# Kernel tuning notes

Measured on AMD Instinct MI355X. Metric: run time of the kernel, lower is better.

Reference implementation:

```python
import jax, jax.numpy as jnp
import numpy as np

D_G = 16384; B = 128; NNZ = 262144
CL1_F = 32; CL1_K = 6; FC1_F = 512; FC2_F = 512
NN_FC1 = 512; NN_FC2 = 256
CL4_F = 32; CL4_K = 4; FC1_G4 = 128; FC2_G4 = 64
OUT = 10; POOL1 = 8; POOL4 = 3; V4 = 10; EMB = 64
FC1FIN = CL1_F * (D_G // POOL1)        # 65536
G4OUT = CL4_F * (OUT // POOL4)         # 96
SUMFIN = FC1_F + NN_FC2 + FC2_G4 + 64  # 896


def _cheby(x, W, b, spmm, K):
    # x: [B, V, Fin]; Chebyshev recursion T_k(L) x with K-order feature stacking
    Bb, V, Fin = x.shape
    x0 = jnp.transpose(x, (1, 2, 0)).reshape(V, Fin * Bb)
    xs = [x0]
    if K > 1:
        x1 = spmm(x0)
        xs.append(x1)
        for _ in range(K - 2):
            x2 = 2.0 * spmm(x1) - x0
            xs.append(x2)
            x0, x1 = x1, x2
    X = jnp.stack(xs).reshape(K, V, Fin, Bb)
    X = jnp.transpose(X, (3, 1, 2, 0)).reshape(Bb * V, Fin * K)  # [B*V, Fin*K]
    return (X @ W.T + b).reshape(Bb, V, -1)


def _gmaxpool(x, p):
    # MaxPool1d(p) over node dim (floor truncation like torch)
    Bb, V, F = x.shape
    Vp = (V // p) * p
    return x[:, :Vp].reshape(Bb, V // p, p, F).max(axis=2)


def setup_inputs():
    key = jax.random.key(0)
    ks = jax.random.split(key, 32)
    def lin(i, fo, fi):
        return (jax.random.normal(ks[i], (fo, fi), jnp.float32) * 0.02,
                jnp.zeros((fo,), jnp.float32))
    cl1_W, cl1_b = lin(0, CL1_F, CL1_K)
    fc1_W, fc1_b = lin(1, FC1_F, FC1FIN)
    fc2_W, fc2_b = lin(2, FC2_F, FC1_F)
    fc3_W, fc3_b = lin(3, D_G, FC2_F)
    nn1_W, nn1_b = lin(4, NN_FC1, D_G)
    nn2_W, nn2_b = lin(5, NN_FC2, NN_FC1)
    cl4_W, cl4_b = lin(6, CL4_F, CL4_K * EMB)
    fcg1_W, fcg1_b = lin(7, FC1_G4, G4OUT)
    fcg2_W, fcg2_b = lin(8, FC2_G4, FC1_G4)
    nn14_W, nn14_b = lin(9, 256, V4 * EMB)
    nn24_W, nn24_b = lin(10, 64, 256)
    fcsum_W, fcsum_b = lin(11, OUT, SUMFIN)
    return {
        'x_in': jax.random.normal(ks[12], (B, D_G), jnp.float32),
        'x_embed': jax.random.normal(ks[13], (V4, EMB), jnp.float32),
        'dropout': 0,
        'L_rows': jnp.sort(jax.random.randint(ks[14], (NNZ,), 0, D_G)),
        'L_cols': jax.random.randint(ks[15], (NNZ,), 0, D_G),
        'L_vals': jax.random.normal(ks[16], (NNZ,), jnp.float32) * 0.1,
        'L_mg': jax.random.normal(ks[17], (V4, V4), jnp.float32) * 0.2,
        'cl1_W': cl1_W, 'cl1_b': cl1_b, 'fc1_W': fc1_W, 'fc1_b': fc1_b,
        'fc2_W': fc2_W, 'fc2_b': fc2_b, 'fc3_W': fc3_W, 'fc3_b': fc3_b,
        'nn1_W': nn1_W, 'nn1_b': nn1_b, 'nn2_W': nn2_W, 'nn2_b': nn2_b,
        'cl4_W': cl4_W, 'cl4_b': cl4_b, 'fcg1_W': fcg1_W, 'fcg1_b': fcg1_b,
        'fcg2_W': fcg2_W, 'fcg2_b': fcg2_b, 'nn14_W': nn14_W, 'nn14_b': nn14_b,
        'nn24_W': nn24_W, 'nn24_b': nn24_b, 'fcsum_W': fcsum_W, 'fcsum_b': fcsum_b,
    }


def reference(x_in, x_embed, dropout, L_rows, L_cols, L_vals, L_mg,
              cl1_W, cl1_b, fc1_W, fc1_b, fc2_W, fc2_b, fc3_W, fc3_b,
              nn1_W, nn1_b, nn2_W, nn2_b, cl4_W, cl4_b,
              fcg1_W, fcg1_b, fcg2_W, fcg2_b, nn14_W, nn14_b, nn24_W, nn24_b,
              fcsum_W, fcsum_b):
    Bb = x_in.shape[0]
    def spmm_L(m):  # COO SpMM: y[r] += v * m[c]
        return jax.ops.segment_sum(L_vals[:, None] * m[L_cols], L_rows,
                                   num_segments=D_G)
    # --- GCN 1 (gene graph) ---
    x = _cheby(x_in[:, :, None], cl1_W, cl1_b, spmm_L, CL1_K)
    x = jax.nn.relu(x)
    x = _gmaxpool(x, POOL1).reshape(Bb, FC1FIN)
    x_hidden_gae = jax.nn.relu(x @ fc1_W.T + fc1_b)
    # FC2_F != 0 branch; dropout p=0 is identity at this baseline
    x_decode_gae = jax.nn.relu(x_hidden_gae @ fc2_W.T + fc2_b)
    x_decode_gae = x_decode_gae @ fc3_W.T + fc3_b
    # --- NN 1 ---
    x_nn = jax.nn.relu(x_in @ nn1_W.T + nn1_b)
    x_nn = jax.nn.relu(x_nn @ nn2_W.T + nn2_b)
    # --- GCN 4 (small meta-graph, dense Laplacian) ---
    xe = jnp.broadcast_to(x_embed[None], (Bb, V4, EMB))
    xg = _cheby(xe, cl4_W, cl4_b, lambda m: L_mg @ m, CL4_K)
    xg = jax.nn.relu(xg)
    xg = _gmaxpool(xg, POOL4).reshape(Bb, G4OUT)
    xg = jax.nn.relu(xg @ fcg1_W.T + fcg1_b)
    xg = jax.nn.relu(xg @ fcg2_W.T + fcg2_b)
    # --- NN of GCN4 ---
    xn4 = xe.reshape(Bb, V4 * EMB)
    xn4 = jax.nn.relu(xn4 @ nn14_W.T + nn14_b)
    xn4 = jax.nn.relu(xn4 @ nn24_W.T + nn24_b)
    data_emb = jnp.concatenate([x_hidden_gae, x_nn, xg, xn4], axis=1)
    logp = jax.nn.log_softmax(data_emb @ fcsum_W.T + fcsum_b, axis=-1)
    return x_decode_gae, x_hidden_gae, logp
```

## Files before the change

### kernel.cpp

```cpp
#include <hip/hip_runtime.h>
#include <hip/hip_bf16.h>

#define DG 16384
#define NNZ 262144
#define BB 128

typedef __attribute__((ext_vector_type(8))) short bf16x8;
typedef __attribute__((ext_vector_type(8))) unsigned short us8;
typedef __attribute__((ext_vector_type(4))) float f32x4;
typedef __attribute__((ext_vector_type(4))) unsigned short us4;
typedef __attribute__((ext_vector_type(2))) float f32x2;

#define WS_ROWPTR 0
#define WS_XIN16  66048
#define WS_T      4260352
#define WS_XPOOL  54592000
#define WS_XB0    71369216
#define WS_XB1    75563520
#define WS_XNN1B  79757824
#define WS_DEC2   79888896
#define WS_XNN2   80019968
#define WS_HIDB   80151040
#define WS_N1     80282112
#define WS_TAIL   80283136
#define PART_NN1_OFF 0
#define PART_FC1_OFF 8388608

__device__ __forceinline__ unsigned short f2bf(float f) {
  __hip_bfloat16 h = __float2bfloat16(f);
  return __builtin_bit_cast(unsigned short, h);
}
__device__ __forceinline__ float bflo(unsigned u) {
  return __builtin_bit_cast(float, u << 16);
}
__device__ __forceinline__ float bfhi(unsigned u) {
  return __builtin_bit_cast(float, u & 0xffff0000u);
}

__device__ void prep_dev(const float* __restrict__ x_in, const int* __restrict__ rows,
                         int* __restrict__ rowptr, unsigned short* __restrict__ xin16,
                         int bid) {
  int idx = bid * 256 + threadIdx.x;
  if (idx <= DG) {
    int lo = 0, hi = NNZ;
    while (lo < hi) { int mid = (lo + hi) >> 1; if (rows[mid] < idx) lo = mid + 1; else hi = mid; }
    rowptr[idx] = lo;
  }
  f32x4 v = ((const f32x4*)x_in)[idx];
  us4 o; o[0] = f2bf(v[0]); o[1] = f2bf(v[1]); o[2] = f2bf(v[2]); o[3] = f2bf(v[3]);
  ((us4*)xin16)[idx] = o;
}

__device__ void transpose_dev(const float* __restrict__ x_in, float* __restrict__ T0,
                              unsigned short* __restrict__ Xb0, int id) {
  __shared__ float tl[32][33];
  int bx = id & 511, by = id >> 9;
  int v0 = bx * 32, b0 = by * 32;
  int tx = threadIdx.x & 31, ty0 = threadIdx.x >> 5;
  #pragma unroll
  for (int j = 0; j < 4; ++j) {
    int ty = ty0 + j * 8;
    tl[ty][tx] = x_in[(size_t)(b0 + ty) * DG + v0 + tx];
  }
  __syncthreads();
  #pragma unroll
  for (int j = 0; j < 4; ++j) {
    int ty = ty0 + j * 8;
    float v = tl[tx][ty];
    size_t o = (size_t)(v0 + ty) * BB + b0 + tx;
    T0[o] = v;
    Xb0[o] = f2bf(v);
  }
}

__device__ void dot4_dev(const float* __restrict__ x, const float* __restrict__ W,
                         const float* __restrict__ bias, float* __restrict__ out,
                         int K, int id) {
  int w = threadIdx.x >> 6, lane = threadIdx.x & 63;
  int o = id * 4 + w;
  float a = 0.f;
  for (int i = lane; i < K; i += 64) a += x[i] * W[(size_t)o * K + i];
  #pragma unroll
  for (int s = 32; s > 0; s >>= 1) a += __shfl_down(a, s);
  if (lane == 0) out[o] = fmaxf(a + bias[o], 0.f);
}

__device__ void g4_dev(const float* __restrict__ xe_g, const float* __restrict__ Lmg_g,
                       const float* __restrict__ W4, const float* __restrict__ b4,
                       const float* __restrict__ Wg1, const float* __restrict__ bg1,
                       const float* __restrict__ Wg2, const float* __restrict__ bg2,
                       float* __restrict__ tail) {
  __shared__ float Lm[100], Tg[4][640], xc[320], xg96[96], h1[128];
  int t = threadIdx.x;
  for (int i = t; i < 640; i += 256) Tg[0][i] = xe_g[i];
  for (int i = t; i < 100; i += 256) Lm[i] = Lmg_g[i];
  __syncthreads();
  for (int i = t; i < 640; i += 256) {
    int v = i >> 6, f = i & 63; float s = 0.f;
    #pragma unroll
    for (int u = 0; u < 10; ++u) s += Lm[v * 10 + u] * Tg[0][u * 64 + f];
    Tg[1][i] = s;
  }
  __syncthreads();
  for (int kk = 2; kk < 4; ++kk) {
    for (int i = t; i < 640; i += 256) {
      int v = i >> 6, f = i & 63; float s = 0.f;
      #pragma unroll
      for (int u = 0; u < 10; ++u) s += Lm[v * 10 + u] * Tg[kk - 1][u * 64 + f];
      Tg[kk][i] = 2.f * s - Tg[kk - 2][i];
    }
    __syncthreads();
  }
  for (int i = t; i < 320; i += 256) {
    int v = i >> 5, fo = i & 31; float s = b4[fo];
    for (int fin = 0; fin < 64; ++fin)
      #pragma unroll
      for (int k = 0; k < 4; ++k) s += Tg[k][v * 64 + fin] * W4[fo * 256 + fin * 4 + k];
    xc[i] = fmaxf(s, 0.f);
  }
  __syncthreads();
  for (int i = t; i < 96; i += 256) {
    int g = i >> 5, fo = i & 31;
    xg96[i] = fmaxf(fmaxf(xc[(3 * g) * 32 + fo], xc[(3 * g + 1) * 32 + fo]),
                    xc[(3 * g + 2) * 32 + fo]);
  }
  __syncthreads();
  for (int o = t; o < 128; o += 256) {
    float s = bg1[o];
    for (int i2 = 0; i2 < 96; ++i2) s += xg96[i2] * Wg1[o * 96 + i2];
    h1[o] = fmaxf(s, 0.f);
  }
  __syncthreads();
  for (int o = t; o < 64; o += 256) {
    float s = bg2[o];
    for (int i2 = 0; i2 < 128; ++i2) s += h1[i2] * Wg2[o * 128 + i2];
    tail[o] = fmaxf(s, 0.f);
  }
}

__global__ __launch_bounds__(256) void setup_kernel(
    const float* __restrict__ x_in, const int* __restrict__ rows,
    int* __restrict__ rowptr, unsigned short* __restrict__ xin16,
    float* __restrict__ T0, unsigned short* __restrict__ Xb0,
    const float* __restrict__ x_embed,
    const float* __restrict__ nn14_W, const float* __restrict__ nn14_b,
    float* __restrict__ n1,
    const float* __restrict__ Lmg, const float* __restrict__ W4,
    const float* __restrict__ b4, const float* __restrict__ Wg1,
    const float* __restrict__ bg1, const float* __restrict__ Wg2,
    const float* __restrict__ bg2, float* __restrict__ tail) {
  int bid = blockIdx.x;
  if (bid < 2048) prep_dev(x_in, rows, rowptr, xin16, bid);
  else if (bid < 4096) transpose_dev(x_in, T0, Xb0, bid - 2048);
  else if (bid < 4160) dot4_dev(x_embed, nn14_W, nn14_b, n1, 640, bid - 4096);
  else g4_dev(x_embed, Lmg, W4, b4, Wg1, bg1, Wg2, bg2, tail);
}

__global__ __launch_bounds__(256) void spmm3(
    const int* __restrict__ rowptr, const int* __restrict__ cols,
    const float* __restrict__ vals, const unsigned* __restrict__ X2,
    const float* __restrict__ Tprev, float* __restrict__ Tout,
    unsigned* __restrict__ Xbout, float scale) {
  int r = blockIdx.x * 4 + (threadIdx.x >> 6);
  int lane = threadIdx.x & 63;
  int e0 = rowptr[r], e1 = rowptr[r + 1];
  float a00 = 0.f, a01 = 0.f, a10 = 0.f, a11 = 0.f;
  int e = e0;
  for (; e + 4 <= e1; e += 4) {
    int c0 = cols[e], c1 = cols[e + 1], c2 = cols[e + 2], c3 = cols[e + 3];
    float v0 = vals[e], v1 = vals[e + 1], v2 = vals[e + 2], v3 = vals[e + 3];
    unsigned x0 = X2[c0 * 64 + lane], x1 = X2[c1 * 64 + lane];
    unsigned x2 = X2[c2 * 64 + lane], x3 = X2[c3 * 64 + lane];
    a00 += v0 * bflo(x0); a10 += v0 * bfhi(x0);
    a01 += v1 * bflo(x1); a11 += v1 * bfhi(x1);
    a00 += v2 * bflo(x2); a10 += v2 * bfhi(x2);
    a01 += v3 * bflo(x3); a11 += v3 * bfhi(x3);
  }
  for (; e < e1; ++e) {
    float v = vals[e]; unsigned x = X2[cols[e] * 64 + lane];
    a00 += v * bflo(x); a10 += v * bfhi(x);
  }
  float s0 = scale * (a00 + a01), s1 = scale * (a10 + a11);
  size_t o = (size_t)r * BB + lane * 2;
  if (Tprev) { f32x2 p = *(const f32x2*)(Tprev + o); s0 -= p[0]; s1 -= p[1]; }
  *(f32x2*)(Tout + o) = (f32x2){s0, s1};
  Xbout[(size_t)r * 64 + lane] = (unsigned)f2bf(s0) | ((unsigned)f2bf(s1) << 16);
}

__device__ void combine_dev(const float* __restrict__ Tbase, const float* __restrict__ W,
                            const float* __restrict__ bias, unsigned short* __restrict__ xpool,
                            int vp) {
  __shared__ float tile[6][8][128];
  __shared__ float Wl[192];
  __shared__ float bl[32];
  for (int i = threadIdx.x; i < 192; i += 256) Wl[i] = W[i];
  if (threadIdx.x < 32) bl[threadIdx.x] = bias[threadIdx.x];
  for (int i = threadIdx.x; i < 6144; i += 256) {
    int k = i >> 10, rem = i & 1023, j = rem >> 7, b = rem & 127;
    tile[k][j][b] = Tbase[(size_t)k * 2097152 + (size_t)(vp * 8 + j) * BB + b];
  }
  __syncthreads();
  for (int p = threadIdx.x; p < 4096; p += 256) {
    int b = p >> 5, f = p & 31;
    float m = -1e30f;
    #pragma unroll
    for (int j = 0; j < 8; ++j) {
      float s = bl[f];
      #pragma unroll
      for (int k = 0; k < 6; ++k) s += tile[k][j][b] * Wl[f * 6 + k];
      m = fmaxf(m, s);
    }
    m = fmaxf(m, 0.f);
    xpool[(size_t)b * 65536 + vp * 32 + f] = f2bf(m);
  }
}

__global__ __launch_bounds__(256) void combine_nn24(
    const float* __restrict__ Tbase, const float* __restrict__ W,
    const float* __restrict__ bias, unsigned short* __restrict__ xpool,
    const float* __restrict__ n1, const float* __restrict__ nn24_W,
    const float* __restrict__ nn24_b, float* __restrict__ tail64) {
  int bid = blockIdx.x;
  if (bid < 2048) combine_dev(Tbase, W, bias, xpool, bid);
  else dot4_dev(n1, nn24_W, nn24_b, tail64, 256, bid - 2048);
}

template<int NT>
__device__ void gemm_core(
    unsigned short* __restrict__ Alds,
    unsigned short* __restrict__ Wlds,
    const unsigned short* __restrict__ A, const float* __restrict__ W,
    float* __restrict__ outP, unsigned short* __restrict__ outB,
    const float* __restrict__ bias, int K, int N, int Kchunk,
    int bx, int by, int relu, int partial) {
  const int CN = NT * 64;
  int t = threadIdx.x, w = t >> 6, lane = t & 63, lr = lane & 15, lg = lane >> 4;
  int n0 = bx * CN;
  int kbeg = by * Kchunk;
  f32x4 acc[8][NT];
  #pragma unroll
  for (int mt = 0; mt < 8; ++mt)
    #pragma unroll
    for (int nt = 0; nt < NT; ++nt)
      acc[mt][nt] = (f32x4){0.f, 0.f, 0.f, 0.f};
  int stages = Kchunk >> 6;
  for (int s = 0; s < stages; ++s) {
    int k0 = kbeg + s * 64;
    #pragma unroll
    for (int j = 0; j < 4; ++j) {
      int idx = j * 256 + t;
      int row = idx >> 3, kk = (idx & 7) * 8;
      us8 v = *(const us8*)(A + (size_t)row * K + k0 + kk);
      *(us8*)(Alds + row * 64 + (kk ^ ((row & 7) << 3))) = v;
    }
    #pragma unroll
    for (int j = 0; j < NT * 4; ++j) {
      int idx = j * 256 + t;
      int wr = idx >> 4, kk = (idx & 15) * 4;
      f32x4 v = *(const f32x4*)(W + (size_t)(n0 + wr) * K + k0 + kk);
      us4 o; o[0] = f2bf(v[0]); o[1] = f2bf(v[1]); o[2] = f2bf(v[2]); o[3] = f2bf(v[3]);
      *(us4*)(Wlds + wr * 64 + (kk ^ ((wr & 7) << 3))) = o;
    }
    __syncthreads();
    #pragma unroll
    for (int h = 0; h < 2; ++h) {
      int k32 = h * 32;
      bf16x8 bfr[NT];
      #pragma unroll
      for (int nt = 0; nt < NT; ++nt) {
        int wrow = w * NT * 16 + nt * 16 + lr;
        bfr[nt] = *(const bf16x8*)(Wlds + wrow * 64 + ((k32 + lg * 8) ^ ((wrow & 7) << 3)));
      }
      #pragma unroll
      for (int mt = 0; mt < 8; ++mt) {
        int arow = mt * 16 + lr;
        bf16x8 af = *(const bf16x8*)(Alds + arow * 64 + ((k32 + lg * 8) ^ ((arow & 7) << 3)));
        #pragma unroll
        for (int nt = 0; nt < NT; ++nt)
          acc[mt][nt] = __builtin_amdgcn_mfma_f32_16x16x32_bf16(af, bfr[nt], acc[mt][nt], 0, 0, 0);
      }
    }
    __syncthreads();
  }
  if (partial) {
    float* P = outP + (size_t)by * 128 * (size_t)N;
    #pragma unroll
    for (int mt = 0; mt < 8; ++mt)
      #pragma unroll
      for (int nt = 0; nt < NT; ++nt) {
        int col = n0 + w * NT * 16 + nt * 16 + lr;
        #pragma unroll
        for (int r2 = 0; r2 < 4; ++r2) {
          int row = mt * 16 + lg * 4 + r2;
          P[(size_t)row * N + col] = acc[mt][nt][r2];
        }
      }
  } else {
    #pragma unroll
    for (int mt = 0; mt < 8; ++mt)
      #pragma unroll
      for (int nt = 0; nt < NT; ++nt) {
        int col = n0 + w * NT * 16 + nt * 16 + lr;
        float bc = bias[col];
        #pragma unroll
        for (int r2 = 0; r2 < 4; ++r2) {
          int row = mt * 16 + lg * 4 + r2;
          float v = acc[mt][nt][r2] + bc;
          if (relu) v = fmaxf(v, 0.f);
          if (outP) outP[(size_t)row * N + col] = v;
          if (outB) outB[(size_t)row * N + col] = f2bf(v);
        }
      }
  }
}

__global__ __launch_bounds__(256) void gemm_partials(
    const unsigned short* __restrict__ xin16, const float* __restrict__ nn1_W,
    const unsigned short* __restrict__ xpool, const float* __restrict__ fc1_W,
    float* __restrict__ pnn1, float* __restrict__ pfc1) {
  __shared__ unsigned short Alds[128 * 64];
  __shared__ unsigned short Wlds[128 * 64];
  int b = blockIdx.x;
  if (b < 128)
    gemm_core<2>(Alds, Wlds, xin16, nn1_W, pnn1, nullptr, nullptr,
                 16384, 512, 512, b & 3, b >> 2, 0, 1);
  else {
    b -= 128;
    gemm_core<2>(Alds, Wlds, xpool, fc1_W, pfc1, nullptr, nullptr,
                 65536, 512, 512, b & 3, b >> 2, 0, 1);
  }
}

__global__ __launch_bounds__(256) void reduce_fused(
    const float* __restrict__ pfc1, const float* __restrict__ fc1_b,
    float* __restrict__ hidden, unsigned short* __restrict__ hidB,
    const float* __restrict__ pnn1, const float* __restrict__ nn1_b,
    unsigned short* __restrict__ xnn1b) {
  int b = blockIdx.x;
  if (b < 256) {
    int idx = b * 256 + threadIdx.x;
    float s = 0.f;
    for (int i = 0; i < 128; ++i) s += pfc1[(size_t)i * 65536 + idx];
    float v = fmaxf(s + fc1_b[idx & 511], 0.f);
    hidden[idx] = v;
    hidB[idx] = f2bf(v);
  } else {
    int idx = (b - 256) * 256 + threadIdx.x;
    float s = 0.f;
    for (int i = 0; i < 32; ++i) s += pnn1[(size_t)i * 65536 + idx];
    float v = fmaxf(s + nn1_b[idx & 511], 0.f);
    xnn1b[idx] = f2bf(v);
  }
}

__global__ __launch_bounds__(256) void fc2nn2_kernel(
    const unsigned short* __restrict__ hidB, const float* __restrict__ fc2_W,
    const float* __restrict__ fc2_b, unsigned short* __restrict__ dec2,
    const unsigned short* __restrict__ xnn1b, const float* __restrict__ nn2_W,
    const float* __restrict__ nn2_b, float* __restrict__ xnn2) {
  __shared__ unsigned short Alds[128 * 64];
  __shared__ unsigned short Wlds[64 * 64];
  int b = blockIdx.x;
  if (b < 8)
    gemm_core<1>(Alds, Wlds, hidB, fc2_W, nullptr, dec2, fc2_b,
                 512, 512, 512, b, 0, 1, 0);
  else
    gemm_core<1>(Alds, Wlds, xnn1b, nn2_W, xnn2, nullptr, nn2_b,
                 512, 256, 512, b - 8, 0, 1, 0);
}

__device__ void fcsum_dev(int id, const float* __restrict__ hidden,
                          const float* __restrict__ xnn2, const float* __restrict__ tail,
                          const float* __restrict__ Ws, const float* __restrict__ bs,
                          float* __restrict__ logp) {
  __shared__ float emb[4][896];
  int w = threadIdx.x >> 6, lane = threadIdx.x & 63;
  int b = id * 4 + w;
  for (int i = lane; i < 896; i += 64)
    emb[w][i] = (i < 512) ? hidden[b * 512 + i]
              : (i < 768) ? xnn2[b * 256 + (i - 512)]
                          : tail[i - 768];
  float l[10];
  #pragma unroll
  for (int o = 0; o < 10; ++o) {
    float a = 0.f;
    for (int i = lane; i < 896; i += 64) a += emb[w][i] * Ws[o * 896 + i];
    #pragma unroll
    for (int s = 32; s > 0; s >>= 1) a += __shfl_down(a, s);
    l[o] = __shfl(a, 0) + bs[o];
  }
  float m = l[0];
  #pragma unroll
  for (int o = 1; o < 10; ++o) m = fmaxf(m, l[o]);
  float sum = 0.f;
  #pragma unroll
  for (int o = 0; o < 10; ++o) sum += expf(l[o] - m);
  float lse = m + logf(sum);
  #pragma unroll
  for (int o = 0; o < 10; ++o)
    if (lane == o) logp[b * 10 + o] = l[o] - lse;
}

__global__ __launch_bounds__(256) void fc3_head(
    const unsigned short* __restrict__ dec2, const float* __restrict__ fc3_W,
    const float* __restrict__ fc3_b, float* __restrict__ out0,
    const float* __restrict__ hidden, const float* __restrict__ xnn2,
    const float* __restrict__ tail, const float* __restrict__ fcsum_W,
    const float* __restrict__ fcsum_b, float* __restrict__ logp) {
  __shared__ unsigned short Alds[128 * 64];
  __shared__ unsigned short Wlds[64 * 64];
  int b = blockIdx.x;
  if (b < 256)
    gemm_core<1>(Alds, Wlds, dec2, fc3_W, out0, nullptr, fc3_b,
                 512, 16384, 512, b, 0, 0, 0);
  else
    fcsum_dev(b - 256, hidden, xnn2, tail, fcsum_W, fcsum_b, logp);
}

extern "C" void kernel_launch(void* const* d_in, const int* in_sizes, int n_in,
                              void* d_out, int out_size, void* d_ws, size_t ws_size,
                              hipStream_t stream) {
  const float* x_in    = (const float*)d_in[0];
  const float* x_embed = (const float*)d_in[1];
  const int*   L_rows  = (const int*)d_in[3];
  const int*   L_cols  = (const int*)d_in[4];
  const float* L_vals  = (const float*)d_in[5];
  const float* L_mg    = (const float*)d_in[6];
  const float* cl1_W = (const float*)d_in[7],  *cl1_b = (const float*)d_in[8];
  const float* fc1_W = (const float*)d_in[9],  *fc1_b = (const float*)d_in[10];
  const float* fc2_W = (const float*)d_in[11], *fc2_b = (const float*)d_in[12];
  const float* fc3_W = (const float*)d_in[13], *fc3_b = (const float*)d_in[14];
  const float* nn1_W = (const float*)d_in[15], *nn1_b = (const float*)d_in[16];
  const float* nn2_W = (const float*)d_in[17], *nn2_b = (const float*)d_in[18];
  const float* cl4_W = (const float*)d_in[19], *cl4_b = (const float*)d_in[20];
  const float* fcg1_W = (const float*)d_in[21], *fcg1_b = (const float*)d_in[22];
  const float* fcg2_W = (const float*)d_in[23], *fcg2_b = (const float*)d_in[24];
  const float* nn14_W = (const float*)d_in[25], *nn14_b = (const float*)d_in[26];
  const float* nn24_W = (const float*)d_in[27], *nn24_b = (const float*)d_in[28];
  const float* fcsum_W = (const float*)d_in[29], *fcsum_b = (const float*)d_in[30];

  char* ws = (char*)d_ws;
  int* rowptr = (int*)(ws + WS_ROWPTR);
  unsigned short* xin16 = (unsigned short*)(ws + WS_XIN16);
  float* T = (float*)(ws + WS_T);
  unsigned short* xpool = (unsigned short*)(ws + WS_XPOOL);
  unsigned short* Xb0 = (unsigned short*)(ws + WS_XB0);
  unsigned short* Xb1 = (unsigned short*)(ws + WS_XB1);
  unsigned short* xnn1b = (unsigned short*)(ws + WS_XNN1B);
  unsigned short* dec2 = (unsigned short*)(ws + WS_DEC2);
  float* xnn2 = (float*)(ws + WS_XNN2);
  unsigned short* hidB = (unsigned short*)(ws + WS_HIDB);
  float* n1 = (float*)(ws + WS_N1);
  float* tail = (float*)(ws + WS_TAIL);
  float* pnn1 = (float*)(ws + WS_T + PART_NN1_OFF);
  float* pfc1 = (float*)(ws + WS_T + PART_FC1_OFF);

  float* out0 = (float*)d_out;
  float* hidden = out0 + 2097152;
  float* logp = out0 + 2097152 + 65536;

  setup_kernel<<<4161, 256, 0, stream>>>(x_in, L_rows, rowptr, xin16, T, Xb0,
                                         x_embed, nn14_W, nn14_b, n1,
                                         L_mg, cl4_W, cl4_b, fcg1_W, fcg1_b,
                                         fcg2_W, fcg2_b, tail);

  spmm3<<<4096, 256, 0, stream>>>(rowptr, L_cols, L_vals, (const unsigned*)Xb0,
                                  nullptr,          T + 1 * 2097152, (unsigned*)Xb1, 1.f);
  spmm3<<<4096, 256, 0, stream>>>(rowptr, L_cols, L_vals, (const unsigned*)Xb1,
                                  T,                T + 2 * 2097152, (unsigned*)Xb0, 2.f);
  spmm3<<<4096, 256, 0, stream>>>(rowptr, L_cols, L_vals, (const unsigned*)Xb0,
                                  T + 1 * 2097152,  T + 3 * 2097152, (unsigned*)Xb1, 2.f);
  spmm3<<<4096, 256, 0, stream>>>(rowptr, L_cols, L_vals, (const unsigned*)Xb1,
                                  T + 2 * 2097152,  T + 4 * 2097152, (unsigned*)Xb0, 2.f);
  spmm3<<<4096, 256, 0, stream>>>(rowptr, L_cols, L_vals, (const unsigned*)Xb0,
                                  T + 3 * 2097152,  T + 5 * 2097152, (unsigned*)Xb1, 2.f);

  combine_nn24<<<2064, 256, 0, stream>>>(T, cl1_W, cl1_b, xpool,
                                         n1, nn24_W, nn24_b, tail + 64);

  gemm_partials<<<640, 256, 0, stream>>>(xin16, nn1_W, xpool, fc1_W, pnn1, pfc1);

  reduce_fused<<<512, 256, 0, stream>>>(pfc1, fc1_b, hidden, hidB,
                                        pnn1, nn1_b, xnn1b);

  fc2nn2_kernel<<<12, 256, 0, stream>>>(hidB, fc2_W, fc2_b, dec2,
                                        xnn1b, nn2_W, nn2_b, xnn2);

  fc3_head<<<288, 256, 0, stream>>>(dec2, fc3_W, fc3_b, out0,
                                    hidden, xnn2, tail, fcsum_W, fcsum_b, logp);
}
```

Baseline: 257.7 us.

## Pre-convert weights to bf16 in spare blocks and register-prefetch GEMM tiles

```diff
diff --git a/kernel.cpp b/kernel.cpp
--- a/kernel.cpp
+++ b/kernel.cpp
@@ -25,6 +25,11 @@
 #define WS_TAIL   80283136
 #define PART_NN1_OFF 0
 #define PART_FC1_OFF 8388608
+#define WS_NN1W16 81000448
+#define WS_FC3W16 97777664
+#define WS_FC2W16 114554880
+#define WS_NN2W16 115079168
+#define WS_FC1W16 115341312
 
 __device__ __forceinline__ unsigned short f2bf(float f) {
   __hip_bfloat16 h = __float2bfloat16(f);
@@ -35,6 +40,17 @@
 }
 __device__ __forceinline__ float bfhi(unsigned u) {
   return __builtin_bit_cast(float, u & 0xffff0000u);
+}
+
+__device__ void conv_dev(const float* __restrict__ src,
+                         unsigned short* __restrict__ dst, int id) {
+  #pragma unroll
+  for (int j = 0; j < 8; ++j) {
+    size_t el = (size_t)id * 8192 + j * 1024 + threadIdx.x * 4;
+    f32x4 v = *(const f32x4*)(src + el);
+    us4 o; o[0] = f2bf(v[0]); o[1] = f2bf(v[1]); o[2] = f2bf(v[2]); o[3] = f2bf(v[3]);
+    *(us4*)(dst + el) = o;
+  }
 }
 
 __device__ void prep_dev(const float* __restrict__ x_in, const int* __restrict__ rows,
@@ -148,19 +164,27 @@
     const float* __restrict__ Lmg, const float* __restrict__ W4,
     const float* __restrict__ b4, const float* __restrict__ Wg1,
     const float* __restrict__ bg1, const float* __restrict__ Wg2,
-    const float* __restrict__ bg2, float* __restrict__ tail) {
+    const float* __restrict__ bg2, float* __restrict__ tail,
+    const float* __restrict__ nn1_W, unsigned short* __restrict__ nn1w16,
+    const float* __restrict__ fc2_W, unsigned short* __restrict__ fc2w16,
+    const float* __restrict__ nn2_W, unsigned short* __restrict__ nn2w16) {
   int bid = blockIdx.x;
-  if (bid < 2048) prep_dev(x_in, rows, rowptr, xin16, bid);
-  else if (bid < 4096) transpose_dev(x_in, T0, Xb0, bid - 2048);
-  else if (bid < 4160) dot4_dev(x_embed, nn14_W, nn14_b, n1, 640, bid - 4096);
-  else g4_dev(x_embed, Lmg, W4, b4, Wg1, bg1, Wg2, bg2, tail);
+  if (bid < 1) g4_dev(x_embed, Lmg, W4, b4, Wg1, bg1, Wg2, bg2, tail);
+  else if (bid < 65) dot4_dev(x_embed, nn14_W, nn14_b, n1, 640, bid - 1);
+  else if (bid < 2113) prep_dev(x_in, rows, rowptr, xin16, bid - 65);
+  else if (bid < 4161) transpose_dev(x_in, T0, Xb0, bid - 2113);
+  else if (bid < 5185) conv_dev(nn1_W, nn1w16, bid - 4161);
+  else if (bid < 5217) conv_dev(fc2_W, fc2w16, bid - 5185);
+  else conv_dev(nn2_W, nn2w16, bid - 5217);
 }
 
 __global__ __launch_bounds__(256) void spmm3(
     const int* __restrict__ rowptr, const int* __restrict__ cols,
     const float* __restrict__ vals, const unsigned* __restrict__ X2,
     const float* __restrict__ Tprev, float* __restrict__ Tout,
-    unsigned* __restrict__ Xbout, float scale) {
+    unsigned* __restrict__ Xbout, float scale,
+    const float* __restrict__ csrc, unsigned short* __restrict__ cdst) {
+  if (blockIdx.x >= 4096) { conv_dev(csrc, cdst, blockIdx.x - 4096); return; }
   int r = blockIdx.x * 4 + (threadIdx.x >> 6);
   int lane = threadIdx.x & 63;
   int e0 = rowptr[r], e1 = rowptr[r + 1];
@@ -225,41 +249,53 @@
   else dot4_dev(n1, nn24_W, nn24_b, tail64, 256, bid - 2048);
 }
 
-template<int NT>
-__device__ void gemm_core(
+template<int NT, int MT>
+__device__ void gemm_core2(
     unsigned short* __restrict__ Alds,
     unsigned short* __restrict__ Wlds,
-    const unsigned short* __restrict__ A, const float* __restrict__ W,
+    const unsigned short* __restrict__ A, const unsigned short* __restrict__ W,
     float* __restrict__ outP, unsigned short* __restrict__ outB,
     const float* __restrict__ bias, int K, int N, int Kchunk,
-    int bx, int by, int relu, int partial) {
-  const int CN = NT * 64;
+    int bx, int by, int row0, int relu, int partial) {
+  const int LA = (MT * 16) / 32;
+  const int LW = (NT * 64) / 32;
   int t = threadIdx.x, w = t >> 6, lane = t & 63, lr = lane & 15, lg = lane >> 4;
-  int n0 = bx * CN;
+  int n0 = bx * NT * 64;
   int kbeg = by * Kchunk;
-  f32x4 acc[8][NT];
-  #pragma unroll
-  for (int mt = 0; mt < 8; ++mt)
-    #pragma unroll
-    for (int nt = 0; nt < NT; ++nt)
-      acc[mt][nt] = (f32x4){0.f, 0.f, 0.f, 0.f};
+  f32x4 acc[MT][NT];
+  #pragma unroll
+  for (int mt = 0; mt < MT; ++mt)
+    #pragma unroll
+    for (int nt = 0; nt < NT; ++nt) acc[mt][nt] = (f32x4){0.f, 0.f, 0.f, 0.f};
+  int rowA[LA], kkA[LA], rowW[LW], kkW[LW];
+  #pragma unroll
+  for (int j = 0; j < LA; ++j) { int idx = j * 256 + t; rowA[j] = idx >> 3; kkA[j] = (idx & 7) * 8; }
+  #pragma unroll
+  for (int j = 0; j < LW; ++j) { int idx = j * 256 + t; rowW[j] = idx >> 3; kkW[j] = (idx & 7) * 8; }
+  us8 ra[LA], rw[LW];
+  #pragma unroll
+  for (int j = 0; j < LA; ++j)
+    ra[j] = *(const us8*)(A + (size_t)(row0 + rowA[j]) * K + kbeg + kkA[j]);
+  #pragma unroll
+  for (int j = 0; j < LW; ++j)
+    rw[j] = *(const us8*)(W + (size_t)(n0 + rowW[j]) * K + kbeg + kkW[j]);
   int stages = Kchunk >> 6;
   for (int s = 0; s < stages; ++s) {
-    int k0 = kbeg + s * 64;
-    #pragma unroll
-    for (int j = 0; j < 4; ++j) {
-      int idx = j * 256 + t;
-      int row = idx >> 3, kk = (idx & 7) * 8;
-      us8 v = *(const us8*)(A + (size_t)row * K + k0 + kk);
-      *(us8*)(Alds + row * 64 + (kk ^ ((row & 7) << 3))) = v;
-    }
-    #pragma unroll
-    for (int j = 0; j < NT * 4; ++j) {
-      int idx = j * 256 + t;
-      int wr = idx >> 4, kk = (idx & 15) * 4;
-      f32x4 v = *(const f32x4*)(W + (size_t)(n0 + wr) * K + k0 + kk);
-      us4 o; o[0] = f2bf(v[0]); o[1] = f2bf(v[1]); o[2] = f2bf(v[2]); o[3] = f2bf(v[3]);
-      *(us4*)(Wlds + wr * 64 + (kk ^ ((wr & 7) << 3))) = o;
+    __syncthreads();
+    #pragma unroll
+    for (int j = 0; j < LA; ++j)
+      *(us8*)(Alds + rowA[j] * 64 + (kkA[j] ^ ((rowA[j] & 7) << 3))) = ra[j];
+    #pragma unroll
+    for (int j = 0; j < LW; ++j)
+      *(us8*)(Wlds + rowW[j] * 64 + (kkW[j] ^ ((rowW[j] & 7) << 3))) = rw[j];
+    if (s + 1 < stages) {
+      int k0 = kbeg + (s + 1) * 64;
+      #pragma unroll
+      for (int j = 0; j < LA; ++j)
+        ra[j] = *(const us8*)(A + (size_t)(row0 + rowA[j]) * K + k0 + kkA[j]);
+      #pragma unroll
+      for (int j = 0; j < LW; ++j)
+        rw[j] = *(const us8*)(W + (size_t)(n0 + rowW[j]) * K + k0 + kkW[j]);
     }
     __syncthreads();
     #pragma unroll
@@ -272,7 +308,7 @@
         bfr[nt] = *(const bf16x8*)(Wlds + wrow * 64 + ((k32 + lg * 8) ^ ((wrow & 7) << 3)));
       }
       #pragma unroll
-      for (int mt = 0; mt < 8; ++mt) {
+      for (int mt = 0; mt < MT; ++mt) {
         int arow = mt * 16 + lr;
         bf16x8 af = *(const bf16x8*)(Alds + arow * 64 + ((k32 + lg * 8) ^ ((arow & 7) << 3)));
         #pragma unroll
@@ -280,31 +316,30 @@
           acc[mt][nt] = __builtin_amdgcn_mfma_f32_16x16x32_bf16(af, bfr[nt], acc[mt][nt], 0, 0, 0);
       }
     }
-    __syncthreads();
   }
   if (partial) {
     float* P = outP + (size_t)by * 128 * (size_t)N;
     #pragma unroll
-    for (int mt = 0; mt < 8; ++mt)
+    for (int mt = 0; mt < MT; ++mt)
       #pragma unroll
       for (int nt = 0; nt < NT; ++nt) {
         int col = n0 + w * NT * 16 + nt * 16 + lr;
         #pragma unroll
         for (int r2 = 0; r2 < 4; ++r2) {
-          int row = mt * 16 + lg * 4 + r2;
+          int row = row0 + mt * 16 + lg * 4 + r2;
           P[(size_t)row * N + col] = acc[mt][nt][r2];
         }
       }
   } else {
     #pragma unroll
-    for (int mt = 0; mt < 8; ++mt)
+    for (int mt = 0; mt < MT; ++mt)
       #pragma unroll
       for (int nt = 0; nt < NT; ++nt) {
         int col = n0 + w * NT * 16 + nt * 16 + lr;
         float bc = bias[col];
         #pragma unroll
         for (int r2 = 0; r2 < 4; ++r2) {
-          int row = mt * 16 + lg * 4 + r2;
+          int row = row0 + mt * 16 + lg * 4 + r2;
           float v = acc[mt][nt][r2] + bc;
           if (relu) v = fmaxf(v, 0.f);
           if (outP) outP[(size_t)row * N + col] = v;
@@ -315,19 +350,21 @@
 }
 
 __global__ __launch_bounds__(256) void gemm_partials(
-    const unsigned short* __restrict__ xin16, const float* __restrict__ nn1_W,
-    const unsigned short* __restrict__ xpool, const float* __restrict__ fc1_W,
+    const unsigned short* __restrict__ xin16, const unsigned short* __restrict__ nn1w16,
+    const unsigned short* __restrict__ xpool, const unsigned short* __restrict__ fc1w16,
     float* __restrict__ pnn1, float* __restrict__ pfc1) {
   __shared__ unsigned short Alds[128 * 64];
   __shared__ unsigned short Wlds[128 * 64];
-  int b = blockIdx.x;
-  if (b < 128)
-    gemm_core<2>(Alds, Wlds, xin16, nn1_W, pnn1, nullptr, nullptr,
-                 16384, 512, 512, b & 3, b >> 2, 0, 1);
-  else {
-    b -= 128;
-    gemm_core<2>(Alds, Wlds, xpool, fc1_W, pfc1, nullptr, nullptr,
-                 65536, 512, 512, b & 3, b >> 2, 0, 1);
+  int nb = blockIdx.x;
+  if (nb < 128) {
+    int xcd = nb & 7, q = nb >> 3, bx = q & 3, by = ((q >> 2) << 3) | xcd;
+    gemm_core2<2, 8>(Alds, Wlds, xin16, nn1w16, pnn1, nullptr, nullptr,
+                     16384, 512, 512, bx, by, 0, 0, 1);
+  } else {
+    int b = nb - 128;
+    int xcd = b & 7, q = b >> 3, bx = q & 3, by = ((q >> 2) << 3) | xcd;
+    gemm_core2<2, 8>(Alds, Wlds, xpool, fc1w16, pfc1, nullptr, nullptr,
+                     65536, 512, 512, bx, by, 0, 0, 1);
   }
 }
 
@@ -354,19 +391,19 @@
 }
 
 __global__ __launch_bounds__(256) void fc2nn2_kernel(
-    const unsigned short* __restrict__ hidB, const float* __restrict__ fc2_W,
+    const unsigned short* __restrict__ hidB, const unsigned short* __restrict__ fc2w16,
     const float* __restrict__ fc2_b, unsigned short* __restrict__ dec2,
-    const unsigned short* __restrict__ xnn1b, const float* __restrict__ nn2_W,
+    const unsigned short* __restrict__ xnn1b, const unsigned short* __restrict__ nn2w16,
     const float* __restrict__ nn2_b, float* __restrict__ xnn2) {
   __shared__ unsigned short Alds[128 * 64];
   __shared__ unsigned short Wlds[64 * 64];
   int b = blockIdx.x;
   if (b < 8)
-    gemm_core<1>(Alds, Wlds, hidB, fc2_W, nullptr, dec2, fc2_b,
-                 512, 512, 512, b, 0, 1, 0);
+    gemm_core2<1, 8>(Alds, Wlds, hidB, fc2w16, nullptr, dec2, fc2_b,
+                     512, 512, 512, b, 0, 0, 1, 0);
   else
-    gemm_core<1>(Alds, Wlds, xnn1b, nn2_W, xnn2, nullptr, nn2_b,
-                 512, 256, 512, b - 8, 0, 1, 0);
+    gemm_core2<1, 8>(Alds, Wlds, xnn1b, nn2w16, xnn2, nullptr, nn2_b,
+                     512, 256, 512, b - 8, 0, 0, 1, 0);
 }
 
 __device__ void fcsum_dev(int id, const float* __restrict__ hidden,
@@ -402,19 +439,21 @@
 }
 
 __global__ __launch_bounds__(256) void fc3_head(
-    const unsigned short* __restrict__ dec2, const float* __restrict__ fc3_W,
+    const unsigned short* __restrict__ dec2, const unsigned short* __restrict__ fc3w16,
     const float* __restrict__ fc3_b, float* __restrict__ out0,
     const float* __restrict__ hidden, const float* __restrict__ xnn2,
     const float* __restrict__ tail, const float* __restrict__ fcsum_W,
     const float* __restrict__ fcsum_b, float* __restrict__ logp) {
-  __shared__ unsigned short Alds[128 * 64];
+  __shared__ unsigned short Alds[64 * 64];
   __shared__ unsigned short Wlds[64 * 64];
   int b = blockIdx.x;
-  if (b < 256)
-    gemm_core<1>(Alds, Wlds, dec2, fc3_W, out0, nullptr, fc3_b,
-                 512, 16384, 512, b, 0, 0, 0);
-  else
-    fcsum_dev(b - 256, hidden, xnn2, tail, fcsum_W, fcsum_b, logp);
+  if (b < 512) {
+    int bx = b >> 1, my = b & 1;
+    gemm_core2<1, 4>(Alds, Wlds, dec2, fc3w16, out0, nullptr, fc3_b,
+                     512, 16384, 512, bx, 0, my * 64, 0, 0);
+  } else {
+    fcsum_dev(b - 512, hidden, xnn2, tail, fcsum_W, fcsum_b, logp);
+  }
 }
 
 extern "C" void kernel_launch(void* const* d_in, const int* in_sizes, int n_in,
@@ -454,38 +493,49 @@
   float* tail = (float*)(ws + WS_TAIL);
   float* pnn1 = (float*)(ws + WS_T + PART_NN1_OFF);
   float* pfc1 = (float*)(ws + WS_T + PART_FC1_OFF);
+  unsigned short* nn1w16 = (unsigned short*)(ws + WS_NN1W16);
+  unsigned short* fc3w16 = (unsigned short*)(ws + WS_FC3W16);
+  unsigned short* fc2w16 = (unsigned short*)(ws + WS_FC2W16);
+  unsigned short* nn2w16 = (unsigned short*)(ws + WS_NN2W16);
+  unsigned short* fc1w16 = (unsigned short*)(ws + WS_FC1W16);
 
   float* out0 = (float*)d_out;
   float* hidden = out0 + 2097152;
   float* logp = out0 + 2097152 + 65536;
 
-  setup_kernel<<<4161, 256, 0, stream>>>(x_in, L_rows, rowptr, xin16, T, Xb0,
+  setup_kernel<<<5233, 256, 0, stream>>>(x_in, L_rows, rowptr, xin16, T, Xb0,
                                          x_embed, nn14_W, nn14_b, n1,
                                          L_mg, cl4_W, cl4_b, fcg1_W, fcg1_b,
-                                         fcg2_W, fcg2_b, tail);
-
-  spmm3<<<4096, 256, 0, stream>>>(rowptr, L_cols, L_vals, (const unsigned*)Xb0,
-                                  nullptr,          T + 1 * 2097152, (unsigned*)Xb1, 1.f);
-  spmm3<<<4096, 256, 0, stream>>>(rowptr, L_cols, L_vals, (const unsigned*)Xb1,
-                                  T,                T + 2 * 2097152, (unsigned*)Xb0, 2.f);
-  spmm3<<<4096, 256, 0, stream>>>(rowptr, L_cols, L_vals, (const unsigned*)Xb0,
-                                  T + 1 * 2097152,  T + 3 * 2097152, (unsigned*)Xb1, 2.f);
-  spmm3<<<4096, 256, 0, stream>>>(rowptr, L_cols, L_vals, (const unsigned*)Xb1,
-                                  T + 2 * 2097152,  T + 4 * 2097152, (unsigned*)Xb0, 2.f);
-  spmm3<<<4096, 256, 0, stream>>>(rowptr, L_cols, L_vals, (const unsigned*)Xb0,
-                                  T + 3 * 2097152,  T + 5 * 2097152, (unsigned*)Xb1, 2.f);
+                                         fcg2_W, fcg2_b, tail,
+                                         nn1_W, nn1w16, fc2_W, fc2w16, nn2_W, nn2w16);
+
+  spmm3<<<5120, 256, 0, stream>>>(rowptr, L_cols, L_vals, (const unsigned*)Xb0,
+                                  nullptr,          T + 1 * 2097152, (unsigned*)Xb1, 1.f,
+                                  fc1_W,            fc1w16);
+  spmm3<<<5120, 256, 0, stream>>>(rowptr, L_cols, L_vals, (const unsigned*)Xb1,
+                                  T,                T + 2 * 2097152, (unsigned*)Xb0, 2.f,
+                                  fc1_W + 8388608,  fc1w16 + 8388608);
+  spmm3<<<5120, 256, 0, stream>>>(rowptr, L_cols, L_vals, (const unsigned*)Xb0,
+                                  T + 1 * 2097152,  T + 3 * 2097152, (unsigned*)Xb1, 2.f,
+                                  fc1_W + 16777216, fc1w16 + 16777216);
+  spmm3<<<5120, 256, 0, stream>>>(rowptr, L_cols, L_vals, (const unsigned*)Xb1,
+                                  T + 2 * 2097152,  T + 4 * 2097152, (unsigned*)Xb0, 2.f,
+                                  fc1_W + 25165824, fc1w16 + 25165824);
+  spmm3<<<5120, 256, 0, stream>>>(rowptr, L_cols, L_vals, (const unsigned*)Xb0,
+                                  T + 3 * 2097152,  T + 5 * 2097152, (unsigned*)Xb1, 2.f,
+                                  fc3_W,            fc3w16);
 
   combine_nn24<<<2064, 256, 0, stream>>>(T, cl1_W, cl1_b, xpool,
                                          n1, nn24_W, nn24_b, tail + 64);
 
-  gemm_partials<<<640, 256, 0, stream>>>(xin16, nn1_W, xpool, fc1_W, pnn1, pfc1);
+  gemm_partials<<<640, 256, 0, stream>>>(xin16, nn1w16, xpool, fc1w16, pnn1, pfc1);
 
   reduce_fused<<<512, 256, 0, stream>>>(pfc1, fc1_b, hidden, hidB,
                                         pnn1, nn1_b, xnn1b);
 
-  fc2nn2_kernel<<<12, 256, 0, stream>>>(hidB, fc2_W, fc2_b, dec2,
-                                        xnn1b, nn2_W, nn2_b, xnn2);
-
-  fc3_head<<<288, 256, 0, stream>>>(dec2, fc3_W, fc3_b, out0,
+  fc2nn2_kernel<<<12, 256, 0, stream>>>(hidB, fc2w16, fc2_b, dec2,
+                                        xnn1b, nn2w16, nn2_b, xnn2);
+
+  fc3_head<<<544, 256, 0, stream>>>(dec2, fc3w16, fc3_b, out0,
                                     hidden, xnn2, tail, fcsum_W, fcsum_b, logp);
 }
```

Result: slower. 286.0 us (+11.0%).
